# Kernel tuning notes

Measured on AMD Instinct MI355X. Metric: run time of the kernel, lower is better.

Reference implementation:

```python
import jax, jax.numpy as jnp
import numpy as np

OUT_FEATURES = 11008
IN_FEATURES = 4096
PACKED_LEN = OUT_FEATURES * IN_FEATURES // 4  # 4 ternary vals per byte, 2 bits each


def setup_inputs() -> dict:
    key = jax.random.key(0)
    k1, k2, k3 = jax.random.split(key, 3)
    x = jax.random.normal(k1, (4, 1024, IN_FEATURES), dtype=jnp.float32)
    packed_weight = jax.random.randint(k2, (PACKED_LEN,), 0, 256, dtype=jnp.int32)
    weight_scale = jax.random.uniform(k3, (1,), dtype=jnp.float32)
    return {"x": x, "packed_weight": packed_weight, "weight_scale": weight_scale}


def _dequantize_weight(packed_weight, weight_scale):
    shifts = jnp.arange(0, 8, 2, dtype=jnp.int32)          # [4]
    q = ((packed_weight[:, None] >> shifts) & 3) - 1        # [P, 4]
    q = q.reshape(OUT_FEATURES, IN_FEATURES).astype(jnp.float32)
    return q * weight_scale.reshape(())                      # dequantize


def reference(x, packed_weight, weight_scale):
    w = _dequantize_weight(packed_weight, weight_scale)      # [out, in]
    # F.linear: y = x @ w.T  (bias=False)
    return jnp.einsum('bsi,oi->bso', x, w)
```

## Files before the change

### kernel.cpp

```cpp
#include <hip/hip_runtime.h>
#include <hip/hip_bf16.h>

#define OUT_F 11008
#define IN_F  4096
#define M_DIM 4096

typedef __attribute__((ext_vector_type(8))) short bf16x8;
typedef __attribute__((ext_vector_type(4))) float f32x4;
typedef __attribute__((ext_vector_type(8))) unsigned short us8;

__device__ __forceinline__ unsigned short f2bf_rne(float f) {
    unsigned u = __builtin_bit_cast(unsigned, f);
    u += 0x7fffu + ((u >> 16) & 1u);
    return (unsigned short)(u >> 16);
}

__global__ void prep_kernel(const float* __restrict__ x,
                            unsigned short* __restrict__ xb,
                            const int* __restrict__ pw,
                            unsigned short* __restrict__ pw2) {
    if (blockIdx.x < 8192) {
        size_t i = ((size_t)blockIdx.x * blockDim.x + threadIdx.x) * 8;
        float4 a = *(const float4*)(x + i);
        float4 b = *(const float4*)(x + i + 4);
        us8 o;
        o[0] = f2bf_rne(a.x); o[1] = f2bf_rne(a.y);
        o[2] = f2bf_rne(a.z); o[3] = f2bf_rne(a.w);
        o[4] = f2bf_rne(b.x); o[5] = f2bf_rne(b.y);
        o[6] = f2bf_rne(b.z); o[7] = f2bf_rne(b.w);
        *(us8*)(xb + i) = o;
    } else {
        __shared__ unsigned char lb[16 * 1028];
        const int rg = blockIdx.x - 8192;
        const int t  = threadIdx.x;
        const int4* src = (const int4*)(pw + (size_t)rg * 16384);
#pragma unroll
        for (int r = 0; r < 16; ++r) {
            int4 v = src[r * 256 + t];
            lb[r * 1028 + t * 4 + 0] = (unsigned char)(v.x & 0xFF);
            lb[r * 1028 + t * 4 + 1] = (unsigned char)(v.y & 0xFF);
            lb[r * 1028 + t * 4 + 2] = (unsigned char)(v.z & 0xFF);
            lb[r * 1028 + t * 4 + 3] = (unsigned char)(v.w & 0xFF);
        }
        __syncthreads();
        unsigned short* dst = pw2 + (size_t)rg * 8192;
#pragma unroll
        for (int i = 0; i < 32; ++i) {
            const int u    = i * 256 + t;
            const int kt   = u >> 7;
            const int h    = (u >> 6) & 1;
            const int qd   = (u >> 4) & 3;
            const int mrow = u & 15;
            const int c0   = kt * 16 + h * 8 + qd * 2;
            dst[u] = (unsigned short)(lb[mrow * 1028 + c0] |
                                      (lb[mrow * 1028 + c0 + 1] << 8));
        }
    }
}

__device__ __forceinline__ void unpack_byte(unsigned b, unsigned& d_lo,
                                            unsigned& d_hi) {
    const unsigned PA = 0x00800080u;
    const unsigned PB = 0x403F00BFu;
    unsigned m0 = (b & 0xFu) * 0x00404101u;
    unsigned s0 = (m0 & 0x03030303u) | 0x00040004u;
    d_lo = __builtin_amdgcn_perm(PA, PB, s0);
    unsigned m1 = (b >> 4) * 0x00404101u;
    unsigned s1 = (m1 & 0x03030303u) | 0x00040004u;
    d_hi = __builtin_amdgcn_perm(PA, PB, s1);
}

__device__ __forceinline__ bf16x8 unpack_us(unsigned short p) {
    unsigned d0, d1, d2, d3;
    unpack_byte(p & 0xFFu, d0, d1);
    unpack_byte((unsigned)p >> 8, d2, d3);
    uint4 u = (uint4){d0, d1, d2, d3};
    return __builtin_bit_cast(bf16x8, u);
}

__global__ __launch_bounds__(512, 2) void gemm_kernel(
    const unsigned short* __restrict__ A,
    const unsigned short* __restrict__ P,
    float* __restrict__ C,
    const float* __restrict__ scale_ptr) {
    constexpr int K  = IN_F;
    constexpr int N  = OUT_F;
    constexpr int NT = K / 64;

    __shared__ unsigned short sA[2][2][256][32];

    const int tid  = threadIdx.x;
    const int wave = tid >> 6;
    const int lane = tid & 63;
    const int quad = lane >> 4;
    const int mrow = lane & 15;
    const int sw   = quad ^ ((mrow >> 1) & 3);

    const int srow = lane >> 2;
    const int sseg = (lane & 3) ^ ((lane >> 3) & 3);

    const int lin = blockIdx.x;
    const int xcd = lin & 7;
    const int q   = lin >> 3;
    const int bm  = xcd * 2 + q / 43;
    const int bn  = q % 43;

    const int wm = (wave >> 2) * 128;
    const int wn = (wave & 3) * 64;

    const unsigned short* Ag = A + (size_t)bm * 256 * K;
    const int rgb = bn * 16 + (wn >> 4);

    f32x4 acc[8][4];
#pragma unroll
    for (int i = 0; i < 8; i++)
#pragma unroll
        for (int j = 0; j < 4; j++) acc[i][j] = (f32x4){0.f, 0.f, 0.f, 0.f};

    auto STAGE_A = [&](int nb, int kbase) {
#pragma unroll
        for (int h = 0; h < 2; ++h) {
#pragma unroll
            for (int c = 0; c < 2; ++c) {
                const int chunk = wave * 2 + c;
                const int grow  = chunk * 16 + srow;
                const unsigned short* src =
                    Ag + (size_t)grow * K + kbase + h * 32 + sseg * 8;
                __builtin_amdgcn_global_load_lds(
                    (const __attribute__((address_space(1))) void*)src,
                    (__attribute__((address_space(3))) void*)
                        (&sA[nb][h][0][0] + chunk * 512),
                    16, 0, 0);
            }
        }
    };

    auto pidx = [&](int kt, int j, int h) -> size_t {
        return (((size_t)(rgb + j) * 64 + kt) * 2 + h) * 64 + lane;
    };

    STAGE_A(0, 0);
    unsigned short pkb[8], npkb[8];
#pragma unroll
    for (int j = 0; j < 4; ++j)
#pragma unroll
        for (int h = 0; h < 2; ++h) pkb[j * 2 + h] = P[pidx(0, j, h)];
#pragma unroll
    for (int i = 0; i < 8; ++i) npkb[i] = 0;
    __syncthreads();

    for (int kt = 0; kt < NT; ++kt) {
        const int  buf  = kt & 1;
        const int  nbuf = buf ^ 1;
        const bool pf1  = (kt + 1 < NT);

        if (pf1) {
            STAGE_A(nbuf, (kt + 1) * 64);
#pragma unroll
            for (int j = 0; j < 4; ++j)
#pragma unroll
                for (int h = 0; h < 2; ++h)
                    npkb[j * 2 + h] = P[pidx(kt + 1, j, h)];
        }

#pragma unroll
        for (int h = 0; h < 2; ++h) {
            bf16x8 a[8], b[4];
#pragma unroll
            for (int j = 0; j < 4; ++j) b[j] = unpack_us(pkb[j * 2 + h]);
#pragma unroll
            for (int t = 0; t < 8; ++t)
                a[t] = *(const bf16x8*)&sA[buf][h][wm + t * 16 + mrow][sw * 8];
#pragma unroll
            for (int t = 0; t < 8; ++t)
#pragma unroll
                for (int j = 0; j < 4; ++j)
                    acc[t][j] = __builtin_amdgcn_mfma_f32_16x16x32_bf16(
                        a[t], b[j], acc[t][j], 0, 0, 0);
        }

#pragma unroll
        for (int i = 0; i < 8; ++i) pkb[i] = npkb[i];

        __syncthreads();
    }

    const float scale = *scale_ptr;
    float* Cg = C + (size_t)(bm * 256 + wm) * N + bn * 256 + wn;
#pragma unroll
    for (int i = 0; i < 8; ++i) {
#pragma unroll
        for (int j = 0; j < 4; ++j) {
#pragma unroll
            for (int r = 0; r < 4; ++r) {
                const int row = i * 16 + quad * 4 + r;
                const int col = j * 16 + mrow;
                Cg[(size_t)row * N + col] = acc[i][j][r] * scale;
            }
        }
    }
}

extern "C" void kernel_launch(void* const* d_in, const int* in_sizes, int n_in,
                              void* d_out, int out_size, void* d_ws, size_t ws_size,
                              hipStream_t stream) {
    const float* x   = (const float*)d_in[0];
    const int* pw    = (const int*)d_in[1];
    const float* wsc = (const float*)d_in[2];

    float* out = (float*)d_out;

    unsigned short* xb  = (unsigned short*)d_ws;
    unsigned short* pw2 = (unsigned short*)((char*)d_ws
                          + (size_t)M_DIM * IN_F * 2);

    prep_kernel<<<8192 + 688, 256, 0, stream>>>(x, xb, pw, pw2);

    gemm_kernel<<<688, 512, 0, stream>>>(xb, pw2, out, wsc);
}
```

Measured before the change: 558.2 us.

## Triple-buffer A tiles and split the K-step into four barrier-separated MFMA phases

Moves the A-tile staging from double to triple buffering in LDS, prefetching two K-steps ahead. Each K-step is split into four quadrant phases, with one async global-to-LDS load issued per phase, explicit s_waitcnt and s_barrier between phases, and s_setprio raised around the MFMA bursts. The aim is to interleave loads, unpacking and matrix math so memory latency is hidden behind compute. In exchange, LDS use grows to 96KB per block, which may cut occupancy below the two blocks requested in launch bounds. The extra barriers and hand-set wait counts also add sync overhead and depend on vmcnt ordering being right.

```diff
diff --git a/kernel.cpp b/kernel.cpp
--- a/kernel.cpp
+++ b/kernel.cpp
@@ -58,6 +58,11 @@
     }
 }
 
+#define LGKM0() do { asm volatile("s_waitcnt lgkmcnt(0)" ::: "memory"); \
+                     __builtin_amdgcn_sched_barrier(0); } while (0)
+#define VMCNT(n) do { asm volatile("s_waitcnt vmcnt(" #n ")" ::: "memory"); \
+                      __builtin_amdgcn_sched_barrier(0); } while (0)
+
 __device__ __forceinline__ void unpack_byte(unsigned b, unsigned& d_lo,
                                             unsigned& d_hi) {
     const unsigned PA = 0x00800080u;
@@ -84,10 +89,10 @@
     float* __restrict__ C,
     const float* __restrict__ scale_ptr) {
     constexpr int K  = IN_F;
-    constexpr int N  = OUT_F;
+    constexpr int NN = OUT_F;
     constexpr int NT = K / 64;
 
-    __shared__ unsigned short sA[2][2][256][32];
+    __shared__ unsigned short sA[3][2][256][32];
 
     const int tid  = threadIdx.x;
     const int wave = tid >> 6;
@@ -110,6 +115,7 @@
 
     const unsigned short* Ag = A + (size_t)bm * 256 * K;
     const int rgb = bn * 16 + (wn >> 4);
+    const unsigned short* Pb = P + (size_t)rgb * 8192 + lane;
 
     f32x4 acc[8][4];
 #pragma unroll
@@ -117,76 +123,138 @@
 #pragma unroll
         for (int j = 0; j < 4; j++) acc[i][j] = (f32x4){0.f, 0.f, 0.f, 0.f};
 
-    auto STAGE_A = [&](int nb, int kbase) {
-#pragma unroll
-        for (int h = 0; h < 2; ++h) {
-#pragma unroll
-            for (int c = 0; c < 2; ++c) {
-                const int chunk = wave * 2 + c;
-                const int grow  = chunk * 16 + srow;
-                const unsigned short* src =
-                    Ag + (size_t)grow * K + kbase + h * 32 + sseg * 8;
-                __builtin_amdgcn_global_load_lds(
-                    (const __attribute__((address_space(1))) void*)src,
-                    (__attribute__((address_space(3))) void*)
-                        (&sA[nb][h][0][0] + chunk * 512),
-                    16, 0, 0);
-            }
-        }
+    auto STAGE_A1 = [&](int nb, int kbase, int part) {
+        const int c = part & 1, h = part >> 1;
+        const int chunk = wave * 2 + c;
+        const int grow  = chunk * 16 + srow;
+        const unsigned short* src =
+            Ag + (size_t)grow * K + kbase + h * 32 + sseg * 8;
+        __builtin_amdgcn_global_load_lds(
+            (const __attribute__((address_space(1))) void*)src,
+            (__attribute__((address_space(3))) void*)
+                (&sA[nb][h][0][0] + chunk * 512),
+            16, 0, 0);
     };
 
-    auto pidx = [&](int kt, int j, int h) -> size_t {
-        return (((size_t)(rgb + j) * 64 + kt) * 2 + h) * 64 + lane;
-    };
-
-    STAGE_A(0, 0);
+#pragma unroll
+    for (int p = 0; p < 4; ++p) STAGE_A1(0, 0, p);
+#pragma unroll
+    for (int p = 0; p < 4; ++p) STAGE_A1(1, 64, p);
     unsigned short pkb[8], npkb[8];
 #pragma unroll
     for (int j = 0; j < 4; ++j)
 #pragma unroll
-        for (int h = 0; h < 2; ++h) pkb[j * 2 + h] = P[pidx(0, j, h)];
+        for (int h = 0; h < 2; ++h)
+            pkb[j * 2 + h] = Pb[(size_t)j * 8192 + h * 64];
 #pragma unroll
     for (int i = 0; i < 8; ++i) npkb[i] = 0;
-    __syncthreads();
+    VMCNT(12);
+    __builtin_amdgcn_s_barrier();
+
+    int bC = 0, bN = 1, bS = 2;
+    bf16x8 a[4][2], b0[2][2], b1[2][2];
 
     for (int kt = 0; kt < NT; ++kt) {
-        const int  buf  = kt & 1;
-        const int  nbuf = buf ^ 1;
-        const bool pf1  = (kt + 1 < NT);
-
+        const bool pf1 = (kt + 1 < NT);
+        const bool pf2 = (kt + 2 < NT);
+        const int  kn2 = (kt + 2) * 64;
+
+#pragma unroll
+        for (int t = 0; t < 4; ++t)
+#pragma unroll
+            for (int h = 0; h < 2; ++h)
+                a[t][h] = *(const bf16x8*)&sA[bC][h][wm + t * 16 + mrow][sw * 8];
+#pragma unroll
+        for (int jj = 0; jj < 2; ++jj)
+#pragma unroll
+            for (int h = 0; h < 2; ++h)
+                b0[jj][h] = unpack_us(pkb[jj * 2 + h]);
+        if (pf2) STAGE_A1(bS, kn2, 0);
+        __builtin_amdgcn_s_barrier();
+        LGKM0();
+        __builtin_amdgcn_s_setprio(1);
+#pragma unroll
+        for (int h = 0; h < 2; ++h)
+#pragma unroll
+            for (int t = 0; t < 4; ++t)
+#pragma unroll
+                for (int jj = 0; jj < 2; ++jj)
+                    acc[t][jj] = __builtin_amdgcn_mfma_f32_16x16x32_bf16(
+                        a[t][h], b0[jj][h], acc[t][jj], 0, 0, 0);
+        __builtin_amdgcn_s_setprio(0);
+        __builtin_amdgcn_s_barrier();
+
+#pragma unroll
+        for (int jj = 0; jj < 2; ++jj)
+#pragma unroll
+            for (int h = 0; h < 2; ++h)
+                b1[jj][h] = unpack_us(pkb[(2 + jj) * 2 + h]);
         if (pf1) {
-            STAGE_A(nbuf, (kt + 1) * 64);
+            const unsigned short* Pk = Pb + (size_t)(kt + 1) * 128;
 #pragma unroll
             for (int j = 0; j < 4; ++j)
 #pragma unroll
                 for (int h = 0; h < 2; ++h)
-                    npkb[j * 2 + h] = P[pidx(kt + 1, j, h)];
-        }
-
-#pragma unroll
-        for (int h = 0; h < 2; ++h) {
-            bf16x8 a[8], b[4];
-#pragma unroll
-            for (int j = 0; j < 4; ++j) b[j] = unpack_us(pkb[j * 2 + h]);
-#pragma unroll
-            for (int t = 0; t < 8; ++t)
-                a[t] = *(const bf16x8*)&sA[buf][h][wm + t * 16 + mrow][sw * 8];
-#pragma unroll
-            for (int t = 0; t < 8; ++t)
-#pragma unroll
-                for (int j = 0; j < 4; ++j)
-                    acc[t][j] = __builtin_amdgcn_mfma_f32_16x16x32_bf16(
-                        a[t], b[j], acc[t][j], 0, 0, 0);
-        }
+                    npkb[j * 2 + h] = Pk[(size_t)j * 8192 + h * 64];
+        }
+        if (pf2) STAGE_A1(bS, kn2, 1);
+        __builtin_amdgcn_s_barrier();
+        LGKM0();
+        __builtin_amdgcn_s_setprio(1);
+#pragma unroll
+        for (int h = 0; h < 2; ++h)
+#pragma unroll
+            for (int t = 0; t < 4; ++t)
+#pragma unroll
+                for (int jj = 0; jj < 2; ++jj)
+                    acc[t][2 + jj] = __builtin_amdgcn_mfma_f32_16x16x32_bf16(
+                        a[t][h], b1[jj][h], acc[t][2 + jj], 0, 0, 0);
+        __builtin_amdgcn_s_setprio(0);
+        __builtin_amdgcn_s_barrier();
+
+#pragma unroll
+        for (int t = 0; t < 4; ++t)
+#pragma unroll
+            for (int h = 0; h < 2; ++h)
+                a[t][h] = *(const bf16x8*)&sA[bC][h][wm + 64 + t * 16 + mrow][sw * 8];
+        if (pf2) STAGE_A1(bS, kn2, 2);
+        __builtin_amdgcn_s_barrier();
+        LGKM0();
+        __builtin_amdgcn_s_setprio(1);
+#pragma unroll
+        for (int h = 0; h < 2; ++h)
+#pragma unroll
+            for (int t = 0; t < 4; ++t)
+#pragma unroll
+                for (int jj = 0; jj < 2; ++jj)
+                    acc[4 + t][2 + jj] = __builtin_amdgcn_mfma_f32_16x16x32_bf16(
+                        a[t][h], b1[jj][h], acc[4 + t][2 + jj], 0, 0, 0);
+        __builtin_amdgcn_s_setprio(0);
+        __builtin_amdgcn_s_barrier();
+
+        if (pf2) STAGE_A1(bS, kn2, 3);
+        __builtin_amdgcn_s_barrier();
+        LGKM0();
+        __builtin_amdgcn_s_setprio(1);
+#pragma unroll
+        for (int h = 0; h < 2; ++h)
+#pragma unroll
+            for (int t = 0; t < 4; ++t)
+#pragma unroll
+                for (int jj = 0; jj < 2; ++jj)
+                    acc[4 + t][jj] = __builtin_amdgcn_mfma_f32_16x16x32_bf16(
+                        a[t][h], b0[jj][h], acc[4 + t][jj], 0, 0, 0);
+        __builtin_amdgcn_s_setprio(0);
 
 #pragma unroll
         for (int i = 0; i < 8; ++i) pkb[i] = npkb[i];
-
-        __syncthreads();
+        VMCNT(12);
+        __builtin_amdgcn_s_barrier();
+        const int t0 = bC; bC = bN; bN = bS; bS = t0;
     }
 
     const float scale = *scale_ptr;
-    float* Cg = C + (size_t)(bm * 256 + wm) * N + bn * 256 + wn;
+    float* Cg = C + (size_t)(bm * 256 + wm) * NN + bn * 256 + wn;
 #pragma unroll
     for (int i = 0; i < 8; ++i) {
 #pragma unroll
@@ -195,7 +263,7 @@
             for (int r = 0; r < 4; ++r) {
                 const int row = i * 16 + quad * 4 + r;
                 const int col = j * 16 + mrow;
-                Cg[(size_t)row * N + col] = acc[i][j][r] * scale;
+                Cg[(size_t)row * NN + col] = acc[i][j][r] * scale;
             }
         }
     }
```

After: 654.4 us. 17.2% more time.
